# Performance work log

Hardware: AMD Instinct MI355X
Metric: run time of the kernel (lower is better)

## Reference

```python
import jax, jax.numpy as jnp
import numpy as np
from jax import lax

B, CIN, IMG, K = 128, 3, 112, 7
C = 1024      # hidden_channels * channel_dilation
HID = 512     # hidden_channels
HW = (IMG // K) ** 2  # 256 patches
EPS = 1e-5


def _prelu(x, a):
    return jnp.where(x > 0, x, a * x)


def _bn(x, g, b):
    # BatchNorm2d with track_running_stats=False: always uses batch stats
    m = x.mean(axis=(0, 2, 3), keepdims=True)
    v = x.var(axis=(0, 2, 3), keepdims=True)
    return (x - m) * lax.rsqrt(v + EPS) * g[None, :, None, None] + b[None, :, None, None]


def setup_inputs() -> dict:
    key = jax.random.key(0)
    ks = jax.random.split(key, 16)
    d = {
        'x':  jax.random.normal(ks[0], (B, CIN, IMG, IMG), jnp.float32),
        'w0': jax.random.normal(ks[1], (C, CIN, K, K), jnp.float32) * 0.05,
        'b0': jax.random.normal(ks[2], (C,), jnp.float32) * 0.01,
        'a0': jnp.full((1,), 0.25, jnp.float32),
    }
    for i in range(1, 4):
        kw, kb = jax.random.split(jax.random.fold_in(key, i))
        d[f'w{i}'] = jax.random.normal(kw, (C, C), jnp.float32) * 0.02
        d[f'b{i}'] = jax.random.normal(kb, (C,), jnp.float32) * 0.01
        d[f'g{i}'] = jnp.ones((C,), jnp.float32)
        d[f'bt{i}'] = jnp.zeros((C,), jnp.float32)
        d[f'p{i}'] = jnp.full((1,), 0.25, jnp.float32)
    d['pos'] = jax.random.normal(ks[3], (1, HW, C), jnp.float32)
    d['am'] = jnp.full((1,), 0.25, jnp.float32)
    d['wm'] = jax.random.normal(ks[4], (HID, C), jnp.float32) * 0.03
    d['bm'] = jax.random.normal(ks[5], (HID,), jnp.float32) * 0.01
    pkeys = jax.random.split(ks[6], B)
    d['perm'] = jax.vmap(lambda k: jax.random.permutation(k, HW))(pkeys).astype(jnp.int32)
    return d


def reference(x, w0, b0, a0,
              w1, b1, g1, bt1, p1,
              w2, b2, g2, bt2, p2,
              w3, b3, g3, bt3, p3,
              pos, am, wm, bm, perm):
    # patch-embed conv: stride = kernel_size -> [B, C, 16, 16]
    h = lax.conv_general_dilated(x, w0, (K, K), 'VALID',
                                 dimension_numbers=('NCHW', 'OIHW', 'NCHW'))
    h = _prelu(h + b0[None, :, None, None], a0)
    for w, b, g, bt, p in ((w1, b1, g1, bt1, p1),
                           (w2, b2, g2, bt2, p2),
                           (w3, b3, g3, bt3, p3)):
        h = jnp.einsum('bchw,dc->bdhw', h, w) + b[None, :, None, None]  # 1x1 conv
        h = _prelu(_bn(h, g, bt), p)
    Bn, Cn, Hn, Wn = h.shape
    enc = h.reshape(Bn, Cn, Hn * Wn).transpose(0, 2, 1)  # [B, HW, C]
    enc = enc + pos                                      # private: add pos embedding
    enc = _prelu(enc, am) @ wm.T + bm                    # mixer -> [B, HW, HID]
    # private: per-sample token permutation (single batched gather)
    return jnp.take_along_axis(enc, perm[:, :, None], axis=1)
```

## Files before the change

kernel.cpp:

```cpp
#include <hip/hip_runtime.h>
#include <hip/hip_bf16.h>
#include <stdint.h>


typedef __attribute__((ext_vector_type(8))) short bf16x8;
typedef __attribute__((ext_vector_type(4))) float f32x4;

__device__ __forceinline__ float bf2f(uint32_t u) {
  union { uint32_t i; float f; } v; v.i = u << 16; return v.f;
}
__device__ __forceinline__ ushort f2bf(float f) {
  union { float f; uint32_t i; } v; v.f = f;
  uint32_t i = v.i;
  return (ushort)((i + 0x7FFFu + ((i >> 16) & 1u)) >> 16);
}

template<int EPI, int XB>
__global__ void __launch_bounds__(256, 2)
gemm_kernel(const ushort* __restrict__ A, const ushort* __restrict__ Bw,
            const float* __restrict__ bias, const float* __restrict__ alpha,
            void* __restrict__ outp, float* __restrict__ part,
            const int* __restrict__ inv, int K, int Dout)
{
  __shared__ __align__(16) ushort At[2][128 * 64];
  __shared__ __align__(16) ushort Bt[2][128 * 64];
  const int tid  = threadIdx.x;
  const int lane = tid & 63;
  const int wid  = tid >> 6;
  const int wm = wid >> 1, wn = wid & 1;

  const int s = blockIdx.x;
  const int j = s >> 3;
  const int x = j & ((1 << XB) - 1);
  const int y = ((j >> XB) << 3) | (s & 7);
  const int t0 = y << 7;
  const int d0 = x << 7;

  f32x4 acc[4][4] = {};

  const int srow   = lane >> 3;
  const int schunk = lane & 7;
  const int NT = K >> 6;

  auto stage = [&](int t, int buf) {
    const int k0 = t << 6;
#pragma unroll
    for (int i = 0; i < 4; ++i) {
      int rbase = (wid << 5) + (i << 3);
      int r = rbase + srow;
      int ca = schunk ^ (r & 7);
      const ushort* ga = A  + (size_t)(t0 + r) * K + k0 + (ca << 3);
      __builtin_amdgcn_global_load_lds(
          (const __attribute__((address_space(1))) uint32_t*)ga,
          (__attribute__((address_space(3))) uint32_t*)(&At[buf][rbase << 6]), 16, 0, 0);
      const ushort* gb = Bw + (size_t)(d0 + r) * K + k0 + (ca << 3);
      __builtin_amdgcn_global_load_lds(
          (const __attribute__((address_space(1))) uint32_t*)gb,
          (__attribute__((address_space(3))) uint32_t*)(&Bt[buf][rbase << 6]), 16, 0, 0);
    }
  };

  stage(0, 0);
  if (NT > 1) stage(1, 1);

  for (int t = 0; t < NT; ++t) {
    const int cur = t & 1;
    if (t + 1 < NT) { asm volatile("s_waitcnt vmcnt(8)" ::: "memory"); }
    else            { asm volatile("s_waitcnt vmcnt(0)" ::: "memory"); }
    __builtin_amdgcn_s_barrier();

    __builtin_amdgcn_s_setprio(1);
#pragma unroll
    for (int kk = 0; kk < 2; ++kk) {
      bf16x8 af[4], bfr[4];
      const int kc = (kk << 2) + (lane >> 4);
#pragma unroll
      for (int m = 0; m < 4; ++m) {
        int row = (wm << 6) + (m << 4) + (lane & 15);
        af[m]  = *(const bf16x8*)&At[cur][(row << 6) + ((kc ^ (row & 7)) << 3)];
        int col = (wn << 6) + (m << 4) + (lane & 15);
        bfr[m] = *(const bf16x8*)&Bt[cur][(col << 6) + ((kc ^ (col & 7)) << 3)];
      }
#pragma unroll
      for (int m = 0; m < 4; ++m)
#pragma unroll
        for (int n = 0; n < 4; ++n)
          acc[m][n] = __builtin_amdgcn_mfma_f32_16x16x32_bf16(af[m], bfr[n], acc[m][n], 0, 0, 0);
    }
    __builtin_amdgcn_s_setprio(0);
    asm volatile("s_waitcnt lgkmcnt(0)" ::: "memory");
    __builtin_amdgcn_s_barrier();
    asm volatile("" ::: "memory");
    if (t + 2 < NT) stage(t + 2, cur);
  }

  float a0 = (EPI == 0) ? alpha[0] : 0.0f;
  float sA[4], s2A[4];
#pragma unroll
  for (int n = 0; n < 4; ++n) { sA[n] = 0.f; s2A[n] = 0.f; }

#pragma unroll
  for (int n = 0; n < 4; ++n) {
    int d = d0 + (wn << 6) + (n << 4) + (lane & 15);
    float bs = bias[d];
#pragma unroll
    for (int m = 0; m < 4; ++m) {
      int tb = t0 + (wm << 6) + (m << 4) + ((lane >> 4) << 2);
#pragma unroll
      for (int r = 0; r < 4; ++r) {
        float v = acc[m][n][r] + bs;
        if (EPI == 0) v = v > 0.f ? v : a0 * v;
        if (EPI == 1) { sA[n] += v; s2A[n] += v * v; }
        if (EPI == 2) {
          int row = tb + r;
          int orow = (row & ~255) | inv[row];
          ((float*)outp)[(size_t)orow * Dout + d] = v;
        } else {
          ((ushort*)outp)[(size_t)(tb + r) * Dout + d] = f2bf(v);
        }
      }
    }
  }

  if (EPI == 1) {
    float2* sm = (float2*)&At[0][0];
    int slot = (wm << 2) | (lane >> 4);
#pragma unroll
    for (int n = 0; n < 4; ++n) {
      int col = (wn << 6) + (n << 4) + (lane & 15);
      sm[slot * 128 + col] = make_float2(sA[n], s2A[n]);
    }
    __syncthreads();
    if (tid < 128) {
      float ss = 0.f, ss2 = 0.f;
      for (int q = 0; q < 8; ++q) {
        float2 v = sm[q * 128 + tid];
        ss += v.x; ss2 += v.y;
      }
      part[(size_t)y * 2048 + d0 + tid]        = ss;
      part[(size_t)y * 2048 + 1024 + d0 + tid] = ss2;
    }
  }
}

__global__ void bnfold_kernel(const float* __restrict__ part, const float* __restrict__ g,
                              const float* __restrict__ bt, float* __restrict__ scsh) {
  int d = (blockIdx.x << 8) + threadIdx.x;
  float s = 0.f, s2 = 0.f;
  for (int j = 0; j < 256; ++j) { s += part[j * 2048 + d]; s2 += part[j * 2048 + 1024 + d]; }
  float mean = s * (1.f / 32768.f);
  float var  = s2 * (1.f / 32768.f) - mean * mean;
  float sc = g[d] * rsqrtf(var + 1e-5f);
  scsh[d] = sc;
  scsh[1024 + d] = bt[d] - mean * sc;
}

template<bool MIX>
__global__ void bnact_kernel(ushort* __restrict__ Y, const float* __restrict__ scsh,
                             const float* __restrict__ p, const float* __restrict__ pos,
                             const float* __restrict__ am) {
  size_t i = (((size_t)blockIdx.x << 8) + threadIdx.x) << 3;
  int d = (int)(i & 1023);
  float pp = p[0];
  float aa = MIX ? am[0] : 0.f;
  float pv[8];
  if (MIX) {
    int prow = (int)((i >> 10) & 255);
    const float4* pb = (const float4*)(pos + ((size_t)prow << 10) + d);
    float4 pA = pb[0], pB = pb[1];
    pv[0]=pA.x; pv[1]=pA.y; pv[2]=pA.z; pv[3]=pA.w;
    pv[4]=pB.x; pv[5]=pB.y; pv[6]=pB.z; pv[7]=pB.w;
  }
  uint4 raw = *(const uint4*)(Y + i);
  uint32_t w[4] = {raw.x, raw.y, raw.z, raw.w};
  uint32_t o[4];
#pragma unroll
  for (int q = 0; q < 4; ++q) {
    int dd = d + q * 2;
    float v0 = bf2f(w[q] & 0xFFFFu) * scsh[dd]     + scsh[1024 + dd];
    float v1 = bf2f(w[q] >> 16)     * scsh[dd + 1] + scsh[1024 + dd + 1];
    v0 = v0 > 0.f ? v0 : pp * v0;
    v1 = v1 > 0.f ? v1 : pp * v1;
    if (MIX) {
      v0 += pv[2 * q];     v1 += pv[2 * q + 1];
      v0 = v0 > 0.f ? v0 : aa * v0;
      v1 = v1 > 0.f ? v1 : aa * v1;
    }
    o[q] = (uint32_t)f2bf(v0) | ((uint32_t)f2bf(v1) << 16);
  }
  *(uint4*)(Y + i) = make_uint4(o[0], o[1], o[2], o[3]);
}

__global__ void invperm_kernel(const int* __restrict__ perm, int* __restrict__ inv) {
  int t = (blockIdx.x << 8) + threadIdx.x;
  inv[(t & ~255) + perm[t]] = t & 255;
}

__global__ void f2b_kernel(const float* __restrict__ in, ushort* __restrict__ out, int n) {
  int i = (blockIdx.x << 8) + threadIdx.x;
  if (i < n) out[i] = f2bf(in[i]);
}

__global__ void padw0_kernel(const float* __restrict__ w0, ushort* __restrict__ o) {
  int d = blockIdx.x, j = threadIdx.x;
  o[d * 192 + j] = (j < 147) ? f2bf(w0[d * 147 + j]) : (ushort)0;
}

__global__ void im2col_kernel(const float* __restrict__ x, ushort* __restrict__ P) {
  int t = blockIdx.x;
  int j = threadIdx.x;
  ushort v = 0;
  if (j < 147) {
    int b = t >> 8, pidx = t & 255;
    int pi = pidx >> 4, pj = pidx & 15;
    int cin = j / 49, rem = j - cin * 49;
    int dy = rem / 7, dx = rem - dy * 7;
    v = f2bf(x[(size_t)(b * 3 + cin) * 12544 + (size_t)(pi * 7 + dy) * 112 + (pj * 7 + dx)]);
  }
  P[(size_t)t * 192 + j] = v;
}

extern "C" void kernel_launch(void* const* d_in, const int* in_sizes, int n_in,
                              void* d_out, int out_size, void* d_ws, size_t ws_size,
                              hipStream_t stream) {
  const float* x   = (const float*)d_in[0];
  const float* w0  = (const float*)d_in[1];
  const float* b0  = (const float*)d_in[2];
  const float* a0  = (const float*)d_in[3];
  const float* w1  = (const float*)d_in[4];
  const float* b1  = (const float*)d_in[5];
  const float* g1  = (const float*)d_in[6];
  const float* bt1 = (const float*)d_in[7];
  const float* p1  = (const float*)d_in[8];
  const float* w2  = (const float*)d_in[9];
  const float* b2  = (const float*)d_in[10];
  const float* g2  = (const float*)d_in[11];
  const float* bt2 = (const float*)d_in[12];
  const float* p2  = (const float*)d_in[13];
  const float* w3  = (const float*)d_in[14];
  const float* b3  = (const float*)d_in[15];
  const float* g3  = (const float*)d_in[16];
  const float* bt3 = (const float*)d_in[17];
  const float* p3  = (const float*)d_in[18];
  const float* pos = (const float*)d_in[19];
  const float* am  = (const float*)d_in[20];
  const float* wm  = (const float*)d_in[21];
  const float* bm  = (const float*)d_in[22];
  const int*  perm = (const int*)d_in[23];

  char* ws = (char*)d_ws;
  ushort* B0   = (ushort*)ws;
  ushort* B1   = (ushort*)(ws + 67108864);
  float*  part = (float*)(ws + 134217728);
  float*  scsh = (float*)(ws + 134217728 + 2097152);
  int*    inv  = (int*)  (ws + 134217728 + 2097152 + 8192);
  ushort* wbuf = (ushort*)(ws + 134217728 + 2097152 + 8192 + 131072);

  invperm_kernel<<<dim3(128), dim3(256), 0, stream>>>(perm, inv);
  im2col_kernel<<<dim3(32768), dim3(192), 0, stream>>>(x, B1);
  padw0_kernel<<<dim3(1024), dim3(192), 0, stream>>>(w0, wbuf);

  gemm_kernel<0, 3><<<dim3(2048), dim3(256), 0, stream>>>(
      B1, wbuf, b0, a0, (void*)B0, nullptr, nullptr, 192, 1024);

  f2b_kernel<<<dim3(4096), dim3(256), 0, stream>>>(w1, wbuf, 1048576);
  gemm_kernel<1, 3><<<dim3(2048), dim3(256), 0, stream>>>(
      B0, wbuf, b1, nullptr, (void*)B1, part, nullptr, 1024, 1024);
  bnfold_kernel<<<dim3(4), dim3(256), 0, stream>>>(part, g1, bt1, scsh);
  bnact_kernel<false><<<dim3(16384), dim3(256), 0, stream>>>(B1, scsh, p1, nullptr, nullptr);

  f2b_kernel<<<dim3(4096), dim3(256), 0, stream>>>(w2, wbuf, 1048576);
  gemm_kernel<1, 3><<<dim3(2048), dim3(256), 0, stream>>>(
      B1, wbuf, b2, nullptr, (void*)B0, part, nullptr, 1024, 1024);
  bnfold_kernel<<<dim3(4), dim3(256), 0, stream>>>(part, g2, bt2, scsh);
  bnact_kernel<false><<<dim3(16384), dim3(256), 0, stream>>>(B0, scsh, p2, nullptr, nullptr);

  f2b_kernel<<<dim3(4096), dim3(256), 0, stream>>>(w3, wbuf, 1048576);
  gemm_kernel<1, 3><<<dim3(2048), dim3(256), 0, stream>>>(
      B0, wbuf, b3, nullptr, (void*)B1, part, nullptr, 1024, 1024);
  bnfold_kernel<<<dim3(4), dim3(256), 0, stream>>>(part, g3, bt3, scsh);
  bnact_kernel<true><<<dim3(16384), dim3(256), 0, stream>>>(B1, scsh, p3, pos, am);

  f2b_kernel<<<dim3(2048), dim3(256), 0, stream>>>(wm, wbuf, 524288);
  gemm_kernel<2, 2><<<dim3(1024), dim3(256), 0, stream>>>(
      B1, wbuf, bm, nullptr, d_out, nullptr, inv, 1024, 512);
}
```

Measured before the change: 457.2 us.

## Enlarge GEMM block tile to 256x256 with 512 threads and 8 waves

The GEMM kernel moves from a 128x128 tile with 4 waves to a 256x256 tile with 8 waves (2x4), each wave computing a 128x64 sub-tile with 32 accumulators. This doubles operand reuse per LDS load and halves global traffic per output. The BN partial-sum layout, the bnfold reduction count and the grid sizes change to match. The patch-embed K is padded from 192 to 256 so it fits the 64-wide K stepping. This raises LDS use to 128 KB per block and increases register pressure, which may limit occupancy. There are also only 512 or 256 blocks, which could leave CUs underused.

```diff
diff --git a/kernel.cpp b/kernel.cpp
--- a/kernel.cpp
+++ b/kernel.cpp
@@ -16,52 +16,51 @@
 }
 
 template<int EPI, int XB>
-__global__ void __launch_bounds__(256, 2)
+__global__ void __launch_bounds__(512, 2)
 gemm_kernel(const ushort* __restrict__ A, const ushort* __restrict__ Bw,
             const float* __restrict__ bias, const float* __restrict__ alpha,
             void* __restrict__ outp, float* __restrict__ part,
             const int* __restrict__ inv, int K, int Dout)
 {
-  __shared__ __align__(16) ushort At[2][128 * 64];
-  __shared__ __align__(16) ushort Bt[2][128 * 64];
+  __shared__ __align__(16) ushort At[2][256 * 64];
+  __shared__ __align__(16) ushort Bt[2][256 * 64];
   const int tid  = threadIdx.x;
   const int lane = tid & 63;
   const int wid  = tid >> 6;
-  const int wm = wid >> 1, wn = wid & 1;
+  const int wm   = wid >> 2;
+  const int wn   = wid & 3;
 
   const int s = blockIdx.x;
   const int j = s >> 3;
   const int x = j & ((1 << XB) - 1);
   const int y = ((j >> XB) << 3) | (s & 7);
-  const int t0 = y << 7;
-  const int d0 = x << 7;
-
-  f32x4 acc[4][4] = {};
-
-  const int srow   = lane >> 3;
-  const int schunk = lane & 7;
+  const int t0 = y << 8;
+  const int d0 = x << 8;
+
+  f32x4 acc[8][4] = {};
+
+  const int lrow8 = lane >> 3;
+  const int csrc  = (lane & 7) ^ lrow8;
   const int NT = K >> 6;
 
   auto stage = [&](int t, int buf) {
     const int k0 = t << 6;
 #pragma unroll
-    for (int i = 0; i < 4; ++i) {
-      int rbase = (wid << 5) + (i << 3);
-      int r = rbase + srow;
-      int ca = schunk ^ (r & 7);
-      const ushort* ga = A  + (size_t)(t0 + r) * K + k0 + (ca << 3);
+    for (int g = 0; g < 4; ++g) {
+      int rb = (g << 6) + (wid << 3);
+      const ushort* ga = A + (size_t)(t0 + rb + lrow8) * K + k0 + (csrc << 3);
       __builtin_amdgcn_global_load_lds(
           (const __attribute__((address_space(1))) uint32_t*)ga,
-          (__attribute__((address_space(3))) uint32_t*)(&At[buf][rbase << 6]), 16, 0, 0);
-      const ushort* gb = Bw + (size_t)(d0 + r) * K + k0 + (ca << 3);
+          (__attribute__((address_space(3))) uint32_t*)(&At[buf][rb << 6]), 16, 0, 0);
+      const ushort* gb = Bw + (size_t)(d0 + rb + lrow8) * K + k0 + (csrc << 3);
       __builtin_amdgcn_global_load_lds(
           (const __attribute__((address_space(1))) uint32_t*)gb,
-          (__attribute__((address_space(3))) uint32_t*)(&Bt[buf][rbase << 6]), 16, 0, 0);
+          (__attribute__((address_space(3))) uint32_t*)(&Bt[buf][rb << 6]), 16, 0, 0);
     }
   };
 
   stage(0, 0);
-  if (NT > 1) stage(1, 1);
+  stage(1, 1);
 
   for (int t = 0; t < NT; ++t) {
     const int cur = t & 1;
@@ -72,17 +71,20 @@
     __builtin_amdgcn_s_setprio(1);
 #pragma unroll
     for (int kk = 0; kk < 2; ++kk) {
-      bf16x8 af[4], bfr[4];
       const int kc = (kk << 2) + (lane >> 4);
-#pragma unroll
-      for (int m = 0; m < 4; ++m) {
-        int row = (wm << 6) + (m << 4) + (lane & 15);
-        af[m]  = *(const bf16x8*)&At[cur][(row << 6) + ((kc ^ (row & 7)) << 3)];
-        int col = (wn << 6) + (m << 4) + (lane & 15);
-        bfr[m] = *(const bf16x8*)&Bt[cur][(col << 6) + ((kc ^ (col & 7)) << 3)];
-      }
-#pragma unroll
-      for (int m = 0; m < 4; ++m)
+      bf16x8 af[8], bfr[4];
+#pragma unroll
+      for (int m = 0; m < 8; ++m) {
+        int row = (wm << 7) + (m << 4) + (lane & 15);
+        af[m] = *(const bf16x8*)&At[cur][(row << 6) + ((kc ^ (row & 7)) << 3)];
+      }
+#pragma unroll
+      for (int n = 0; n < 4; ++n) {
+        int col = (wn << 6) + (n << 4) + (lane & 15);
+        bfr[n] = *(const bf16x8*)&Bt[cur][(col << 6) + ((kc ^ (col & 7)) << 3)];
+      }
+#pragma unroll
+      for (int m = 0; m < 8; ++m)
 #pragma unroll
         for (int n = 0; n < 4; ++n)
           acc[m][n] = __builtin_amdgcn_mfma_f32_16x16x32_bf16(af[m], bfr[n], acc[m][n], 0, 0, 0);
@@ -94,7 +96,7 @@
     if (t + 2 < NT) stage(t + 2, cur);
   }
 
-  float a0 = (EPI == 0) ? alpha[0] : 0.0f;
+  float a0v = (EPI == 0) ? alpha[0] : 0.0f;
   float sA[4], s2A[4];
 #pragma unroll
   for (int n = 0; n < 4; ++n) { sA[n] = 0.f; s2A[n] = 0.f; }
@@ -104,12 +106,12 @@
     int d = d0 + (wn << 6) + (n << 4) + (lane & 15);
     float bs = bias[d];
 #pragma unroll
-    for (int m = 0; m < 4; ++m) {
-      int tb = t0 + (wm << 6) + (m << 4) + ((lane >> 4) << 2);
+    for (int m = 0; m < 8; ++m) {
+      int tb = t0 + (wm << 7) + (m << 4) + ((lane >> 4) << 2);
 #pragma unroll
       for (int r = 0; r < 4; ++r) {
         float v = acc[m][n][r] + bs;
-        if (EPI == 0) v = v > 0.f ? v : a0 * v;
+        if (EPI == 0) v = v > 0.f ? v : a0v * v;
         if (EPI == 1) { sA[n] += v; s2A[n] += v * v; }
         if (EPI == 2) {
           int row = tb + r;
@@ -127,14 +129,14 @@
     int slot = (wm << 2) | (lane >> 4);
 #pragma unroll
     for (int n = 0; n < 4; ++n) {
-      int col = (wn << 6) + (n << 4) + (lane & 15);
-      sm[slot * 128 + col] = make_float2(sA[n], s2A[n]);
+      int c = (wn << 6) + (n << 4) + (lane & 15);
+      sm[slot * 256 + c] = make_float2(sA[n], s2A[n]);
     }
     __syncthreads();
-    if (tid < 128) {
+    if (tid < 256) {
       float ss = 0.f, ss2 = 0.f;
       for (int q = 0; q < 8; ++q) {
-        float2 v = sm[q * 128 + tid];
+        float2 v = sm[q * 256 + tid];
         ss += v.x; ss2 += v.y;
       }
       part[(size_t)y * 2048 + d0 + tid]        = ss;
@@ -147,7 +149,7 @@
                               const float* __restrict__ bt, float* __restrict__ scsh) {
   int d = (blockIdx.x << 8) + threadIdx.x;
   float s = 0.f, s2 = 0.f;
-  for (int j = 0; j < 256; ++j) { s += part[j * 2048 + d]; s2 += part[j * 2048 + 1024 + d]; }
+  for (int j = 0; j < 128; ++j) { s += part[j * 2048 + d]; s2 += part[j * 2048 + 1024 + d]; }
   float mean = s * (1.f / 32768.f);
   float var  = s2 * (1.f / 32768.f) - mean * mean;
   float sc = g[d] * rsqrtf(var + 1e-5f);
@@ -203,7 +205,7 @@
 
 __global__ void padw0_kernel(const float* __restrict__ w0, ushort* __restrict__ o) {
   int d = blockIdx.x, j = threadIdx.x;
-  o[d * 192 + j] = (j < 147) ? f2bf(w0[d * 147 + j]) : (ushort)0;
+  o[d * 256 + j] = (j < 147) ? f2bf(w0[d * 147 + j]) : (ushort)0;
 }
 
 __global__ void im2col_kernel(const float* __restrict__ x, ushort* __restrict__ P) {
@@ -217,7 +219,7 @@
     int dy = rem / 7, dx = rem - dy * 7;
     v = f2bf(x[(size_t)(b * 3 + cin) * 12544 + (size_t)(pi * 7 + dy) * 112 + (pj * 7 + dx)]);
   }
-  P[(size_t)t * 192 + j] = v;
+  P[(size_t)t * 256 + j] = v;
 }
 
 extern "C" void kernel_launch(void* const* d_in, const int* in_sizes, int n_in,
@@ -257,31 +259,31 @@
   ushort* wbuf = (ushort*)(ws + 134217728 + 2097152 + 8192 + 131072);
 
   invperm_kernel<<<dim3(128), dim3(256), 0, stream>>>(perm, inv);
-  im2col_kernel<<<dim3(32768), dim3(192), 0, stream>>>(x, B1);
-  padw0_kernel<<<dim3(1024), dim3(192), 0, stream>>>(w0, wbuf);
-
-  gemm_kernel<0, 3><<<dim3(2048), dim3(256), 0, stream>>>(
-      B1, wbuf, b0, a0, (void*)B0, nullptr, nullptr, 192, 1024);
+  im2col_kernel<<<dim3(32768), dim3(256), 0, stream>>>(x, B1);
+  padw0_kernel<<<dim3(1024), dim3(256), 0, stream>>>(w0, wbuf);
+
+  gemm_kernel<0, 2><<<dim3(512), dim3(512), 0, stream>>>(
+      B1, wbuf, b0, a0, (void*)B0, nullptr, nullptr, 256, 1024);
 
   f2b_kernel<<<dim3(4096), dim3(256), 0, stream>>>(w1, wbuf, 1048576);
-  gemm_kernel<1, 3><<<dim3(2048), dim3(256), 0, stream>>>(
+  gemm_kernel<1, 2><<<dim3(512), dim3(512), 0, stream>>>(
       B0, wbuf, b1, nullptr, (void*)B1, part, nullptr, 1024, 1024);
   bnfold_kernel<<<dim3(4), dim3(256), 0, stream>>>(part, g1, bt1, scsh);
   bnact_kernel<false><<<dim3(16384), dim3(256), 0, stream>>>(B1, scsh, p1, nullptr, nullptr);
 
   f2b_kernel<<<dim3(4096), dim3(256), 0, stream>>>(w2, wbuf, 1048576);
-  gemm_kernel<1, 3><<<dim3(2048), dim3(256), 0, stream>>>(
+  gemm_kernel<1, 2><<<dim3(512), dim3(512), 0, stream>>>(
       B1, wbuf, b2, nullptr, (void*)B0, part, nullptr, 1024, 1024);
   bnfold_kernel<<<dim3(4), dim3(256), 0, stream>>>(part, g2, bt2, scsh);
   bnact_kernel<false><<<dim3(16384), dim3(256), 0, stream>>>(B0, scsh, p2, nullptr, nullptr);
 
   f2b_kernel<<<dim3(4096), dim3(256), 0, stream>>>(w3, wbuf, 1048576);
-  gemm_kernel<1, 3><<<dim3(2048), dim3(256), 0, stream>>>(
+  gemm_kernel<1, 2><<<dim3(512), dim3(512), 0, stream>>>(
       B0, wbuf, b3, nullptr, (void*)B1, part, nullptr, 1024, 1024);
   bnfold_kernel<<<dim3(4), dim3(256), 0, stream>>>(part, g3, bt3, scsh);
   bnact_kernel<true><<<dim3(16384), dim3(256), 0, stream>>>(B1, scsh, p3, pos, am);
 
   f2b_kernel<<<dim3(2048), dim3(256), 0, stream>>>(wm, wbuf, 524288);
-  gemm_kernel<2, 2><<<dim3(1024), dim3(256), 0, stream>>>(
+  gemm_kernel<2, 1><<<dim3(256), dim3(512), 0, stream>>>(
       B1, wbuf, bm, nullptr, d_out, nullptr, inv, 1024, 512);
 }
```

Measured after the change: 468.4 us. +2.4%, slower.
